# Performance work log

Measured on AMD Instinct MI355X. Metric: run time of the kernel, lower is better.

## Reference

```python
import jax, jax.numpy as jnp
import numpy as np

B, S, I, H, O = 64, 4096, 256, 256, 128


def setup_inputs() -> dict:
    key = jax.random.key(0)
    ks = jax.random.split(key, 7)
    s_in = 1.0 / np.sqrt(I)
    s_h = 1.0 / np.sqrt(H)
    return {
        "x": jax.random.normal(ks[0], (B, S, I), dtype=jnp.float32),
        "Wax_w": jax.random.uniform(ks[1], (H, I), jnp.float32, -s_in, s_in),
        "Wax_b": jax.random.uniform(ks[2], (H,), jnp.float32, -s_in, s_in),
        "Waa_w": jax.random.uniform(ks[3], (H, H), jnp.float32, -s_h, s_h),
        "Waa_b": jax.random.uniform(ks[4], (H,), jnp.float32, -s_h, s_h),
        "Wya_w": jax.random.uniform(ks[5], (O, H), jnp.float32, -s_h, s_h),
        "Wya_b": jax.random.uniform(ks[6], (O,), jnp.float32, -s_h, s_h),
    }


def reference(x, Wax_w, Wax_b, Waa_w, Waa_b, Wya_w, Wya_b):
    # Precompute input projections for all timesteps in one big GEMM: [B,S,H]
    xp = jnp.einsum("bsi,hi->bsh", x, Wax_w) + Wax_b

    def step(a_prev, xp_t):
        a_next = jnp.tanh(xp_t + a_prev @ Waa_w.T + Waa_b)
        return a_next, None

    a0 = jnp.zeros((x.shape[0], Waa_w.shape[0]), dtype=x.dtype)
    a_last, _ = jax.lax.scan(step, a0, jnp.swapaxes(xp, 0, 1))  # scan over S
    return jax.nn.sigmoid(a_last @ Wya_w.T + Wya_b)
```

## Files before the change

### kernel.cpp

```cpp
#include <hip/hip_runtime.h>
#include <hip/hip_fp16.h>


typedef _Float16 f16x8 __attribute__((ext_vector_type(8)));
typedef _Float16 f16x4 __attribute__((ext_vector_type(4)));
typedef _Float16 f16x2 __attribute__((ext_vector_type(2)));
typedef float    f32x4 __attribute__((ext_vector_type(4)));

#define FDOT2(a, b, c) __builtin_amdgcn_fdot2((a), (b), (c), false)

template <int D>
__device__ __forceinline__ float rorf(float v) {
    return __builtin_bit_cast(float,
        __builtin_amdgcn_update_dpp(0, __builtin_bit_cast(int, v),
                                    0x120 + D, 0xF, 0xF, true));
}

__global__ __launch_bounds__(512)
__attribute__((amdgpu_waves_per_eu(2, 2)))
void k_fused(
    const float* __restrict__ x, const float* __restrict__ Ww,
    const float* __restrict__ Wb, const float* __restrict__ Waa,
    const float* __restrict__ Wab, const float* __restrict__ Wya,
    const float* __restrict__ Wyb, float* __restrict__ out,
    _Float16* __restrict__ xp0, _Float16* __restrict__ xp1,
    unsigned short* __restrict__ a_state,
    int c_rnn, int c_xp, int do_rnn, int do_xp, int is_last,
    int T_C, int logT)
{
    __shared__ __align__(16) _Float16 As[64 * 264];
    __shared__ __align__(16) _Float16 aL[2][16][24];
    __shared__ float afin[256];

    const int tid  = threadIdx.x;
    const int lane = tid & 63;

    if (blockIdx.x < 64) {
        if (!do_rnn) return;
        const _Float16* xp = (c_rnn & 1) ? xp1 : xp0;
        const int w     = tid >> 6;
        const int k     = lane & 15;
        const int g     = lane >> 4;
        const int rbase = w * 32 + g * 8;
        const int myrow = rbase + (k & 7);
        const int b     = blockIdx.x;
        const bool wlane = (k & 8) == 0;

        f16x2 wr[8][8];
#pragma unroll
        for (int i = 0; i < 8; ++i) {
            const float4* wp = (const float4*)(Waa + (size_t)(rbase + ((k + i) & 7)) * 256 + k * 16);
#pragma unroll
            for (int q = 0; q < 4; ++q) {
                float4 v = wp[q];
                f16x2 t0; t0[0] = (_Float16)v.x; t0[1] = (_Float16)v.y;
                f16x2 t1; t1[0] = (_Float16)v.z; t1[1] = (_Float16)v.w;
                wr[i][2 * q]     = t0;
                wr[i][2 * q + 1] = t1;
            }
        }
        const float bias = Wab[myrow];

        if (tid < 256) {
            unsigned short v = 0;
            if (c_rnn != 0) v = a_state[b * 256 + tid];
            aL[0][tid >> 4][tid & 15] = __builtin_bit_cast(_Float16, v);
        }
        __syncthreads();

        const _Float16* xph = xp + ((size_t)(b * 256 + myrow)) * T_C;
        f16x8 xq = *(const f16x8*)(xph);
        float bx[8];
#pragma unroll
        for (int j = 0; j < 8; ++j) bx[j] = bias + (float)xq[j];

        const _Float16* rp0 = &aL[0][k][0];
        const _Float16* rp1 = &aL[1][k][0];
        _Float16* wq0 = &aL[1][myrow >> 4][myrow & 15];
        _Float16* wq1 = &aL[0][myrow >> 4][myrow & 15];

#define RNN_STEP(J, FIN)                                                     \
    {                                                                        \
        const _Float16* rp = ((J) & 1) ? rp1 : rp0;                          \
        uint4 r0 = *(const uint4*)(rp);                                      \
        uint4 r1 = *(const uint4*)(rp + 8);                                  \
        f16x2 a2[8];                                                         \
        a2[0] = __builtin_bit_cast(f16x2, r0.x);                             \
        a2[1] = __builtin_bit_cast(f16x2, r0.y);                             \
        a2[2] = __builtin_bit_cast(f16x2, r0.z);                             \
        a2[3] = __builtin_bit_cast(f16x2, r0.w);                             \
        a2[4] = __builtin_bit_cast(f16x2, r1.x);                             \
        a2[5] = __builtin_bit_cast(f16x2, r1.y);                             \
        a2[6] = __builtin_bit_cast(f16x2, r1.z);                             \
        a2[7] = __builtin_bit_cast(f16x2, r1.w);                             \
        float s0 = 0.f, s1 = 0.f, s2 = 0.f, s3 = 0.f;                        \
        float s4 = 0.f, s5 = 0.f, s6 = 0.f, s7 = 0.f;                        \
        _Pragma("unroll")                                                    \
        for (int q = 0; q < 8; ++q) {                                        \
            s0 = FDOT2(wr[0][q], a2[q], s0);                                 \
            s1 = FDOT2(wr[1][q], a2[q], s1);                                 \
            s2 = FDOT2(wr[2][q], a2[q], s2);                                 \
            s3 = FDOT2(wr[3][q], a2[q], s3);                                 \
            s4 = FDOT2(wr[4][q], a2[q], s4);                                 \
            s5 = FDOT2(wr[5][q], a2[q], s5);                                 \
            s6 = FDOT2(wr[6][q], a2[q], s6);                                 \
            s7 = FDOT2(wr[7][q], a2[q], s7);                                 \
        }                                                                    \
                                                  \
        float p0 = s0 + rorf<8>(s0);                                         \
        float p1 = s1 + rorf<8>(s1);                                         \
        float p2 = s2 + rorf<8>(s2);                                         \
        float p3 = s3 + rorf<8>(s3);                                         \
        float p4 = s4 + rorf<8>(s4);                                         \
        float p5 = s5 + rorf<8>(s5);                                         \
        float p6 = s6 + rorf<8>(s6);                                         \
        float p7 = s7 + rorf<8>(s7);                                         \
        float q0 = p0 + rorf<4>(p4);                                         \
        float q1 = p1 + rorf<4>(p5);                                         \
        float q2 = p2 + rorf<4>(p6);                                         \
        float q3 = p3 + rorf<4>(p7);                                         \
        float acc = (q0 + rorf<1>(q1)) + (rorf<2>(q2) + rorf<3>(q3));        \
        float z  = bx[(J)] + acc;                                            \
        float e2 = __expf(2.f * z);                                          \
        float a  = fmaf(-2.f, __builtin_amdgcn_rcpf(e2 + 1.f), 1.f);         \
        _Float16 ah = (_Float16)a;                                           \
        if (wlane) *(((J) & 1) ? wq1 : wq0) = ah;                            \
        if (FIN) {                                                           \
            afin[myrow] = a;                                                 \
            a_state[b * 256 + myrow] = __builtin_bit_cast(unsigned short, ah);\
        }                                                                    \
        asm volatile("s_waitcnt lgkmcnt(0)" ::: "memory");                   \
        __builtin_amdgcn_s_barrier();                                        \
        asm volatile("" ::: "memory");                                       \
    }

        for (int tb = 0; tb + 8 < T_C; tb += 8) {
            f16x8 xn = *(const f16x8*)(xph + tb + 8);
            RNN_STEP(0, false) RNN_STEP(1, false) RNN_STEP(2, false) RNN_STEP(3, false)
            RNN_STEP(4, false) RNN_STEP(5, false) RNN_STEP(6, false) RNN_STEP(7, false)
#pragma unroll
            for (int j = 0; j < 8; ++j) bx[j] = bias + (float)xn[j];
        }
        RNN_STEP(0, false) RNN_STEP(1, false) RNN_STEP(2, false) RNN_STEP(3, false)
        RNN_STEP(4, false) RNN_STEP(5, false) RNN_STEP(6, false) RNN_STEP(7, true)
#undef RNN_STEP

        if (is_last) {
            const int o  = tid >> 2;
            const int k4 = tid & 3;
            const float4* wp = (const float4*)(Wya + (size_t)o * 256 + k4 * 64);
            const float4* ap = (const float4*)(afin + k4 * 64);
            float s = 0.f;
#pragma unroll
            for (int i = 0; i < 16; ++i) {
                float4 wv4 = wp[i];
                float4 a4  = ap[i];
                s += wv4.x * a4.x + wv4.y * a4.y + wv4.z * a4.z + wv4.w * a4.w;
            }
            s += __shfl_xor(s, 1);
            s += __shfl_xor(s, 2);
            if (k4 == 0)
                out[b * 128 + o] = __builtin_amdgcn_rcpf(1.f + __expf(-(s + Wyb[o])));
        }
    } else {
        if (!do_xp) return;
        _Float16* xp = (c_xp & 1) ? xp1 : xp0;
        const int bxp = blockIdx.x - 64;
        const int wv  = tid >> 6;
        const int l15 = lane & 15;
        const int lk  = lane >> 4;
        const int n0  = wv * 32;

        f16x8 bfr[2][8];
#pragma unroll
        for (int nt = 0; nt < 2; ++nt) {
            const float* wrow = Ww + (size_t)(n0 + nt * 16 + l15) * 256;
#pragma unroll
            for (int kt = 0; kt < 8; ++kt) {
                const float4* wp = (const float4*)(wrow + kt * 32 + lk * 8);
                float4 v0 = wp[0], v1 = wp[1];
                f16x8 f;
                f[0] = (_Float16)v0.x; f[1] = (_Float16)v0.y;
                f[2] = (_Float16)v0.z; f[3] = (_Float16)v0.w;
                f[4] = (_Float16)v1.x; f[5] = (_Float16)v1.y;
                f[6] = (_Float16)v1.z; f[7] = (_Float16)v1.w;
                bfr[nt][kt] = f;
            }
        }
        const float bias0 = Wb[n0 + l15];
        const float bias1 = Wb[n0 + 16 + l15];

        {
            const int arow = tid >> 3;
            const int acol = (tid & 7) * 32;
            const int r    = bxp * 64 + arow;
            const int bb   = r >> logT;
            const int tl   = r & (T_C - 1);
            const float4* s4 = (const float4*)(x + ((size_t)(bb * 4096 + c_xp * T_C + tl) << 8) + acol);
            _Float16* d = As + arow * 264 + acol;
#pragma unroll
            for (int q = 0; q < 4; ++q) {
                float4 v0 = s4[2 * q], v1 = s4[2 * q + 1];
                f16x8 p;
                p[0] = (_Float16)v0.x; p[1] = (_Float16)v0.y;
                p[2] = (_Float16)v0.z; p[3] = (_Float16)v0.w;
                p[4] = (_Float16)v1.x; p[5] = (_Float16)v1.y;
                p[6] = (_Float16)v1.z; p[7] = (_Float16)v1.w;
                *(f16x8*)(d + q * 8) = p;
            }
        }
        __syncthreads();

        f32x4 acc[4][2] = {};
#pragma unroll
        for (int kt = 0; kt < 8; ++kt) {
#pragma unroll
            for (int mt = 0; mt < 4; ++mt) {
                f16x8 af = *(const f16x8*)(As + (mt * 16 + l15) * 264 + kt * 32 + lk * 8);
                acc[mt][0] = __builtin_amdgcn_mfma_f32_16x16x32_f16(af, bfr[0][kt], acc[mt][0], 0, 0, 0);
                acc[mt][1] = __builtin_amdgcn_mfma_f32_16x16x32_f16(af, bfr[1][kt], acc[mt][1], 0, 0, 0);
            }
        }

        const int base = bxp * 64;
#pragma unroll
        for (int mt = 0; mt < 4; ++mt) {
            const int rr  = base + mt * 16 + lk * 4;
            const int bb2 = rr >> logT;
            const int tt  = rr & (T_C - 1);
#pragma unroll
            for (int nt = 0; nt < 2; ++nt) {
                const int   h    = n0 + nt * 16 + l15;
                const float bias = (nt == 0) ? bias0 : bias1;
                f16x4 pk;
#pragma unroll
                for (int r2 = 0; r2 < 4; ++r2) pk[r2] = (_Float16)(acc[mt][nt][r2] + bias);
                *(f16x4*)(xp + ((size_t)(bb2 * 256 + h)) * T_C + tt) = pk;
            }
        }
    }
}

extern "C" void kernel_launch(void* const* d_in, const int* in_sizes, int n_in,
                              void* d_out, int out_size, void* d_ws, size_t ws_size,
                              hipStream_t stream)
{
    (void)in_sizes; (void)n_in; (void)out_size;
    const float* x    = (const float*)d_in[0];
    const float* Waxw = (const float*)d_in[1];
    const float* Waxb = (const float*)d_in[2];
    const float* Waaw = (const float*)d_in[3];
    const float* Waab = (const float*)d_in[4];
    const float* Wyaw = (const float*)d_in[5];
    const float* Wyab = (const float*)d_in[6];
    float* out = (float*)d_out;

    int T_C = 1024, logT = 10;
    while (T_C > 128 && (size_t)2 * 64 * T_C * 256 * 2 + 32768 > ws_size) { T_C >>= 1; --logT; }

    _Float16* xp0 = (_Float16*)d_ws;
    _Float16* xp1 = xp0 + (size_t)64 * T_C * 256;
    unsigned short* a_state = (unsigned short*)(xp1 + (size_t)64 * T_C * 256);

    const int nc  = 4096 / T_C;
    const int nxp = T_C;
    for (int i = 0; i <= nc; ++i) {
        k_fused<<<dim3(64 + nxp), dim3(512), 0, stream>>>(
            x, Waxw, Waxb, Waaw, Waab, Wyaw, Wyab, out, xp0, xp1, a_state,
            i - 1, i, i >= 1 ? 1 : 0, i < nc ? 1 : 0, i == nc ? 1 : 0,
            T_C, logT);
    }
}
```

Baseline: 1.913 ms.

## Compute recurrent matvec with MFMA instead of fdot2 and DPP reductions

Measured after the change: 2.629 ms. 37.4% more time.

```diff
diff --git a/kernel.cpp b/kernel.cpp
--- a/kernel.cpp
+++ b/kernel.cpp
@@ -4,17 +4,7 @@
 
 typedef _Float16 f16x8 __attribute__((ext_vector_type(8)));
 typedef _Float16 f16x4 __attribute__((ext_vector_type(4)));
-typedef _Float16 f16x2 __attribute__((ext_vector_type(2)));
 typedef float    f32x4 __attribute__((ext_vector_type(4)));
-
-#define FDOT2(a, b, c) __builtin_amdgcn_fdot2((a), (b), (c), false)
-
-template <int D>
-__device__ __forceinline__ float rorf(float v) {
-    return __builtin_bit_cast(float,
-        __builtin_amdgcn_update_dpp(0, __builtin_bit_cast(int, v),
-                                    0x120 + D, 0xF, 0xF, true));
-}
 
 __global__ __launch_bounds__(512)
 __attribute__((amdgpu_waves_per_eu(2, 2)))
@@ -29,7 +19,7 @@
     int T_C, int logT)
 {
     __shared__ __align__(16) _Float16 As[64 * 264];
-    __shared__ __align__(16) _Float16 aL[2][16][24];
+    __shared__ __align__(16) _Float16 aB[2][264];
     __shared__ float afin[256];
 
     const int tid  = threadIdx.x;
@@ -38,96 +28,86 @@
     if (blockIdx.x < 64) {
         if (!do_rnn) return;
         const _Float16* xp = (c_rnn & 1) ? xp1 : xp0;
-        const int w     = tid >> 6;
-        const int k     = lane & 15;
-        const int g     = lane >> 4;
-        const int rbase = w * 32 + g * 8;
-        const int myrow = rbase + (k & 7);
-        const int b     = blockIdx.x;
-        const bool wlane = (k & 8) == 0;
-
-        f16x2 wr[8][8];
-#pragma unroll
-        for (int i = 0; i < 8; ++i) {
-            const float4* wp = (const float4*)(Waa + (size_t)(rbase + ((k + i) & 7)) * 256 + k * 16);
-#pragma unroll
-            for (int q = 0; q < 4; ++q) {
-                float4 v = wp[q];
-                f16x2 t0; t0[0] = (_Float16)v.x; t0[1] = (_Float16)v.y;
-                f16x2 t1; t1[0] = (_Float16)v.z; t1[1] = (_Float16)v.w;
-                wr[i][2 * q]     = t0;
-                wr[i][2 * q + 1] = t1;
-            }
-        }
-        const float bias = Wab[myrow];
+        const int w   = tid >> 6;
+        const int l15 = lane & 15;
+        const int g   = lane >> 4;
+        const int b   = blockIdx.x;
+        const bool wl = (l15 == 0);
+
+        f16x8 wa[2][8];
+#pragma unroll
+        for (int t = 0; t < 2; ++t) {
+            const float* wrow = Waa + (size_t)(w * 32 + t * 16 + l15) * 256 + g * 8;
+#pragma unroll
+            for (int kt = 0; kt < 8; ++kt) {
+                const float4* wp = (const float4*)(wrow + kt * 32);
+                float4 v0 = wp[0], v1 = wp[1];
+                f16x8 f;
+                f[0] = (_Float16)v0.x; f[1] = (_Float16)v0.y;
+                f[2] = (_Float16)v0.z; f[3] = (_Float16)v0.w;
+                f[4] = (_Float16)v1.x; f[5] = (_Float16)v1.y;
+                f[6] = (_Float16)v1.z; f[7] = (_Float16)v1.w;
+                wa[t][kt] = f;
+            }
+        }
 
         if (tid < 256) {
             unsigned short v = 0;
             if (c_rnn != 0) v = a_state[b * 256 + tid];
-            aL[0][tid >> 4][tid & 15] = __builtin_bit_cast(_Float16, v);
+            aB[0][tid] = __builtin_bit_cast(_Float16, v);
         }
         __syncthreads();
 
-        const _Float16* xph = xp + ((size_t)(b * 256 + myrow)) * T_C;
-        f16x8 xq = *(const f16x8*)(xph);
-        float bx[8];
-#pragma unroll
-        for (int j = 0; j < 8; ++j) bx[j] = bias + (float)xq[j];
-
-        const _Float16* rp0 = &aL[0][k][0];
-        const _Float16* rp1 = &aL[1][k][0];
-        _Float16* wq0 = &aL[1][myrow >> 4][myrow & 15];
-        _Float16* wq1 = &aL[0][myrow >> 4][myrow & 15];
-
-#define RNN_STEP(J, FIN)                                                     \
+        const _Float16* xph[8];
+#pragma unroll
+        for (int s = 0; s < 8; ++s) {
+            const int row = w * 32 + (s >> 2) * 16 + g * 4 + (s & 3);
+            xph[s] = xp + ((size_t)(b * 256 + row)) * T_C;
+        }
+        f16x8 xq[8], xn[8];
+#pragma unroll
+        for (int s = 0; s < 8; ++s) xq[s] = *(const f16x8*)(xph[s]);
+
+        const int row0 = w * 32 + g * 4;
+        const int row1 = row0 + 16;
+
+#define RNN_STEP(P, J, FIN)                                                  \
     {                                                                        \
-        const _Float16* rp = ((J) & 1) ? rp1 : rp0;                          \
-        uint4 r0 = *(const uint4*)(rp);                                      \
-        uint4 r1 = *(const uint4*)(rp + 8);                                  \
-        f16x2 a2[8];                                                         \
-        a2[0] = __builtin_bit_cast(f16x2, r0.x);                             \
-        a2[1] = __builtin_bit_cast(f16x2, r0.y);                             \
-        a2[2] = __builtin_bit_cast(f16x2, r0.z);                             \
-        a2[3] = __builtin_bit_cast(f16x2, r0.w);                             \
-        a2[4] = __builtin_bit_cast(f16x2, r1.x);                             \
-        a2[5] = __builtin_bit_cast(f16x2, r1.y);                             \
-        a2[6] = __builtin_bit_cast(f16x2, r1.z);                             \
-        a2[7] = __builtin_bit_cast(f16x2, r1.w);                             \
-        float s0 = 0.f, s1 = 0.f, s2 = 0.f, s3 = 0.f;                        \
-        float s4 = 0.f, s5 = 0.f, s6 = 0.f, s7 = 0.f;                        \
+        const _Float16* bp = &aB[(P)][g * 8];                                \
+        f32x4 c0 = {0.f, 0.f, 0.f, 0.f}, c1 = {0.f, 0.f, 0.f, 0.f};          \
         _Pragma("unroll")                                                    \
-        for (int q = 0; q < 8; ++q) {                                        \
-            s0 = FDOT2(wr[0][q], a2[q], s0);                                 \
-            s1 = FDOT2(wr[1][q], a2[q], s1);                                 \
-            s2 = FDOT2(wr[2][q], a2[q], s2);                                 \
-            s3 = FDOT2(wr[3][q], a2[q], s3);                                 \
-            s4 = FDOT2(wr[4][q], a2[q], s4);                                 \
-            s5 = FDOT2(wr[5][q], a2[q], s5);                                 \
-            s6 = FDOT2(wr[6][q], a2[q], s6);                                 \
-            s7 = FDOT2(wr[7][q], a2[q], s7);                                 \
+        for (int kt = 0; kt < 8; ++kt) {                                     \
+            f16x8 bf = *(const f16x8*)(bp + kt * 32);                        \
+            c0 = __builtin_amdgcn_mfma_f32_16x16x32_f16(wa[0][kt], bf, c0, 0, 0, 0); \
+            c1 = __builtin_amdgcn_mfma_f32_16x16x32_f16(wa[1][kt], bf, c1, 0, 0, 0); \
         }                                                                    \
-                                                  \
-        float p0 = s0 + rorf<8>(s0);                                         \
-        float p1 = s1 + rorf<8>(s1);                                         \
-        float p2 = s2 + rorf<8>(s2);                                         \
-        float p3 = s3 + rorf<8>(s3);                                         \
-        float p4 = s4 + rorf<8>(s4);                                         \
-        float p5 = s5 + rorf<8>(s5);                                         \
-        float p6 = s6 + rorf<8>(s6);                                         \
-        float p7 = s7 + rorf<8>(s7);                                         \
-        float q0 = p0 + rorf<4>(p4);                                         \
-        float q1 = p1 + rorf<4>(p5);                                         \
-        float q2 = p2 + rorf<4>(p6);                                         \
-        float q3 = p3 + rorf<4>(p7);                                         \
-        float acc = (q0 + rorf<1>(q1)) + (rorf<2>(q2) + rorf<3>(q3));        \
-        float z  = bx[(J)] + acc;                                            \
-        float e2 = __expf(2.f * z);                                          \
-        float a  = fmaf(-2.f, __builtin_amdgcn_rcpf(e2 + 1.f), 1.f);         \
-        _Float16 ah = (_Float16)a;                                           \
-        if (wlane) *(((J) & 1) ? wq1 : wq0) = ah;                            \
-        if (FIN) {                                                           \
-            afin[myrow] = a;                                                 \
-            a_state[b * 256 + myrow] = __builtin_bit_cast(unsigned short, ah);\
+        f16x4 o0, o1;                                                        \
+        float a0v[4], a1v[4];                                                \
+        _Pragma("unroll")                                                    \
+        for (int r = 0; r < 4; ++r) {                                        \
+            float z0 = c0[r] + (float)xq[r][(J)];                            \
+            float e0 = __expf(2.f * z0);                                     \
+            a0v[r] = fmaf(-2.f, __builtin_amdgcn_rcpf(e0 + 1.f), 1.f);       \
+            o0[r] = (_Float16)a0v[r];                                        \
+            float z1 = c1[r] + (float)xq[4 + r][(J)];                        \
+            float e1 = __expf(2.f * z1);                                     \
+            a1v[r] = fmaf(-2.f, __builtin_amdgcn_rcpf(e1 + 1.f), 1.f);       \
+            o1[r] = (_Float16)a1v[r];                                        \
+        }                                                                    \
+        if (wl) {                                                            \
+            *(f16x4*)&aB[(P) ^ 1][row0] = o0;                                \
+            *(f16x4*)&aB[(P) ^ 1][row1] = o1;                                \
+            if (FIN) {                                                       \
+                _Pragma("unroll")                                            \
+                for (int r = 0; r < 4; ++r) {                                \
+                    afin[row0 + r] = a0v[r];                                 \
+                    afin[row1 + r] = a1v[r];                                 \
+                    a_state[b * 256 + row0 + r] =                            \
+                        __builtin_bit_cast(unsigned short, o0[r]);           \
+                    a_state[b * 256 + row1 + r] =                            \
+                        __builtin_bit_cast(unsigned short, o1[r]);           \
+                }                                                            \
+            }                                                                \
         }                                                                    \
         asm volatile("s_waitcnt lgkmcnt(0)" ::: "memory");                   \
         __builtin_amdgcn_s_barrier();                                        \
@@ -135,14 +115,19 @@
     }
 
         for (int tb = 0; tb + 8 < T_C; tb += 8) {
-            f16x8 xn = *(const f16x8*)(xph + tb + 8);
-            RNN_STEP(0, false) RNN_STEP(1, false) RNN_STEP(2, false) RNN_STEP(3, false)
-            RNN_STEP(4, false) RNN_STEP(5, false) RNN_STEP(6, false) RNN_STEP(7, false)
-#pragma unroll
-            for (int j = 0; j < 8; ++j) bx[j] = bias + (float)xn[j];
-        }
-        RNN_STEP(0, false) RNN_STEP(1, false) RNN_STEP(2, false) RNN_STEP(3, false)
-        RNN_STEP(4, false) RNN_STEP(5, false) RNN_STEP(6, false) RNN_STEP(7, true)
+#pragma unroll
+            for (int s = 0; s < 8; ++s) xn[s] = *(const f16x8*)(xph[s] + tb + 8);
+            RNN_STEP(0, 0, false) RNN_STEP(1, 1, false)
+            RNN_STEP(0, 2, false) RNN_STEP(1, 3, false)
+            RNN_STEP(0, 4, false) RNN_STEP(1, 5, false)
+            RNN_STEP(0, 6, false) RNN_STEP(1, 7, false)
+#pragma unroll
+            for (int s = 0; s < 8; ++s) xq[s] = xn[s];
+        }
+        RNN_STEP(0, 0, false) RNN_STEP(1, 1, false)
+        RNN_STEP(0, 2, false) RNN_STEP(1, 3, false)
+        RNN_STEP(0, 4, false) RNN_STEP(1, 5, false)
+        RNN_STEP(0, 6, false) RNN_STEP(1, 7, true)
 #undef RNN_STEP
 
         if (is_last) {
@@ -187,8 +172,8 @@
                 bfr[nt][kt] = f;
             }
         }
-        const float bias0 = Wb[n0 + l15];
-        const float bias1 = Wb[n0 + 16 + l15];
+        const float bias0 = Wb[n0 + l15]      + Wab[n0 + l15];
+        const float bias1 = Wb[n0 + 16 + l15] + Wab[n0 + 16 + l15];
 
         {
             const int arow = tid >> 3;
```
